# Optimization experiments

Measured on AMD Instinct MI355X. Metric: run time of the kernel, lower is better.

The kernel has to match this reference:

```python
import jax, jax.numpy as jnp
import numpy as np

K = 20      # kNN neighbours (hardcoded in DGCNN)
RES = 64    # 3D grid resolution


def setup_inputs() -> dict:
    key = jax.random.key(0)
    k1, k2 = jax.random.split(key)
    pts = jax.random.uniform(k1, (4, 4096, 3), dtype=jnp.float32)    # point coords in (0,1)
    query = jax.random.uniform(k2, (4, 8192, 3), dtype=jnp.float32)  # query coords in (0,1)
    return {"pts": pts, "query": query}


def _graph_feature(pts, k):
    # pts: (B, N, 3). Faithful to knn() + get_graph_feature(): topk of negative
    # squared pairwise distance (includes self), gather neighbours, cat(nbr - x, x),
    # then max-pool over the k neighbours (standard EdgeConv reduction).
    sq = jnp.sum(pts * pts, axis=-1)                          # (B, N)
    inner = jnp.einsum('bnd,bmd->bnm', pts, pts)              # (B, N, N)
    neg_dist = 2.0 * inner - sq[:, :, None] - sq[:, None, :]  # -||xi - xj||^2
    _, idx = jax.lax.top_k(neg_dist, k)                       # (B, N, k)
    nbr = jax.vmap(lambda p, i: p[i])(pts, idx)               # (B, N, k, 3) gather
    central = jnp.broadcast_to(pts[:, :, None, :], nbr.shape)
    feat = jnp.concatenate([nbr - central, central], axis=-1)  # (B, N, k, 6)
    return jnp.max(feat, axis=2)                               # (B, N, 6)


def _corners(pts, res):
    # Trilinear corner indices and weights, faithful to point_rasterize / grid_interp.
    size = jnp.float32(res)
    ind0 = jnp.floor(pts * size).astype(jnp.int32)                       # (B, P, 3)
    ind1 = jnp.mod(jnp.ceil(pts * size), size).astype(jnp.int32)         # wrap-around
    com = jnp.stack(jnp.meshgrid(*([jnp.arange(2)] * 3), indexing='ij'),
                    axis=-1).reshape(-1, 3)                              # (8, 3) corner combos
    pick1 = (com[None, None] != 0)                                       # (1, 1, 8, 3)
    ind_n = jnp.where(pick1, ind1[:, :, None, :], ind0[:, :, None, :])   # (B, P, 8, 3)
    xyz0 = ind0.astype(pts.dtype) / size
    xyz1 = (ind0.astype(pts.dtype) + 1.0) / size
    # opposite corner position (torch: xyz01[1 - com_])
    pos_opp = jnp.where(pick1, xyz0[:, :, None, :], xyz1[:, :, None, :])
    w = jnp.prod(jnp.abs(pts[:, :, None, :] - pos_opp) * size, axis=-1)  # (B, P, 8)
    return ind_n, w


def _rasterize(pts, vals, res):
    # pts: (B, N, 3), vals: (B, N, F) -> grid (B, res, res, res, F) via scatter-add.
    B, _, F = vals.shape
    ind_n, w = _corners(pts, res)
    flat = (ind_n[..., 0] * res + ind_n[..., 1]) * res + ind_n[..., 2]   # (B, N, 8)
    contrib = w[..., None] * vals[:, :, None, :]                          # (B, N, 8, F)

    def one(fl, c):
        return jnp.zeros((res * res * res, F), vals.dtype).at[fl.reshape(-1)].add(
            c.reshape(-1, F))

    grid = jax.vmap(one)(flat, contrib)                                   # (B, res^3, F)
    return grid.reshape(B, res, res, res, F)


def _grid_interp(grid, q, res):
    # grid: (B, res, res, res, F), q: (B, M, 3) -> (B, M, F)
    ind_n, w = _corners(q, res)

    def one(g, i):
        return g[i[..., 0], i[..., 1], i[..., 2]]   # (M, 8, F) gather

    lat = jax.vmap(one)(grid, ind_n)
    return jnp.sum(lat * w[..., None], axis=-2)


def reference(pts, query):
    feat = _graph_feature(pts, K)            # (B, N, 6)  kNN graph-feature gather
    grid = _rasterize(pts, feat, RES)        # (B, R, R, R, 6) trilinear scatter
    out = _grid_interp(grid, query, RES)     # (B, M, 6)  trilinear gather
    return out
```

## Files before the change

kernel.cpp:

```cpp
#include <hip/hip_runtime.h>

#define BATCH 4
#define NPTS  4096
#define NQ    8192
#define KNN   20
#define RES   64
#define FDIM  6
#define BN    (BATCH * NPTS)

#define WPB   16
#define CAP   128
#define R0 0.1551f

#define GRID_ELEMS ((size_t)BATCH * RES * RES * RES * FDIM)
#define GRID_BYTES (GRID_ELEMS * sizeof(float))

__device__ __forceinline__ float dist2s(float cx, float cy, float cz,
                                        float px, float py, float pz) {
    float dx = cx - px, dy = cy - py, dz = cz - pz;
    return __builtin_fmaf(dz, dz, __builtin_fmaf(dy, dy, dx * dx));
}

__global__ __launch_bounds__(1024) void knn_kernel(const float* __restrict__ pts,
                                                   float* __restrict__ feat) {
    __shared__ float sh[NPTS * 3];
    __shared__ float cd2[WPB][CAP];
    __shared__ unsigned short cidx[WPB][CAP];

    const int tid  = threadIdx.x;
    const int w    = tid >> 6;
    const int lane = tid & 63;
    const int pgrp = blockIdx.x % (NPTS / WPB);
    const int b    = blockIdx.x / (NPTS / WPB);
    const int pi   = pgrp * WPB + w;
    const int pt   = b * NPTS + pi;

    {
        const float4* src = (const float4*)(pts + (size_t)b * NPTS * 3);
        float4* dst = (float4*)sh;
        dst[tid]        = src[tid];
        dst[tid + 1024] = src[tid + 1024];
        dst[tid + 2048] = src[tid + 2048];
    }
    __syncthreads();

    const float px = sh[pi * 3 + 0];
    const float py = sh[pi * 3 + 1];
    const float pz = sh[pi * 3 + 2];

    float r = R0;
    #pragma unroll
    for (int it = 0; it < 2; ++it) {
        float ex = fminf(px + r, 1.f) - fmaxf(px - r, 0.f);
        float ey = fminf(py + r, 1.f) - fmaxf(py - r, 0.f);
        float ez = fminf(pz + r, 1.f) - fmaxf(pz - r, 0.f);
        float frac = (ex * ey * ez) / (8.f * r * r * r);
        r = R0 * __powf(frac, -1.f / 3.f);
    }
    r *= 1.05f;
    const float tau = r * r;

    float*          wd2 = cd2[w];
    unsigned short* wid = cidx[w];
    int total = 0;
    for (int it = 0; it < 64; ++it) {
        const int j = (it << 6) + lane;
        float d2 = dist2s(sh[j * 3 + 0], sh[j * 3 + 1], sh[j * 3 + 2], px, py, pz);
        bool pred = d2 <= tau;
        unsigned long long m = __ballot(pred);
        int before = __builtin_amdgcn_mbcnt_hi((unsigned)(m >> 32),
                     __builtin_amdgcn_mbcnt_lo((unsigned)m, 0));
        int slot = total + before;
        if (pred && slot < CAP) { wd2[slot] = d2; wid[slot] = (unsigned short)j; }
        total += __popcll(m);
    }

    float gx = -3.4e38f, gy = -3.4e38f, gz = -3.4e38f;
    const bool ok = (total >= KNN) && (total <= CAP);

    if (ok) {
        unsigned u0 = (lane < total)      ? __float_as_uint(wd2[lane])      : 0x7F800000u;
        unsigned u1 = (lane + 64 < total) ? __float_as_uint(wd2[lane + 64]) : 0x7F800000u;
        unsigned lo = 0u, hi = __float_as_uint(tau);
        while (lo < hi) {
            unsigned mid = (lo + hi) >> 1;
            int c = __popcll(__ballot(u0 <= mid)) + __popcll(__ballot(u1 <= mid));
            if (c >= KNN) hi = mid; else lo = mid + 1;
        }
        const unsigned tb = hi;
        if (u0 <= tb) {
            int j = wid[lane];
            gx = fmaxf(gx, sh[j * 3 + 0]); gy = fmaxf(gy, sh[j * 3 + 1]); gz = fmaxf(gz, sh[j * 3 + 2]);
        }
        if (u1 <= tb) {
            int j = wid[lane + 64];
            gx = fmaxf(gx, sh[j * 3 + 0]); gy = fmaxf(gy, sh[j * 3 + 1]); gz = fmaxf(gz, sh[j * 3 + 2]);
        }
    } else {
        unsigned lo = 0u, hi = 0x7F7FFFFFu;
        while (lo < hi) {
            unsigned mid = (lo + hi) >> 1;
            int c = 0;
            for (int it = 0; it < 64; ++it) {
                const int j = (it << 6) + lane;
                float d2 = dist2s(sh[j * 3 + 0], sh[j * 3 + 1], sh[j * 3 + 2], px, py, pz);
                c += __popcll(__ballot(__float_as_uint(d2) <= mid));
            }
            if (c >= KNN) hi = mid; else lo = mid + 1;
        }
        const unsigned tb = hi;
        for (int it = 0; it < 64; ++it) {
            const int j = (it << 6) + lane;
            float d2 = dist2s(sh[j * 3 + 0], sh[j * 3 + 1], sh[j * 3 + 2], px, py, pz);
            if (__float_as_uint(d2) <= tb) {
                gx = fmaxf(gx, sh[j * 3 + 0]); gy = fmaxf(gy, sh[j * 3 + 1]); gz = fmaxf(gz, sh[j * 3 + 2]);
            }
        }
    }

    #pragma unroll
    for (int dlt = 1; dlt < 64; dlt <<= 1) {
        gx = fmaxf(gx, __shfl_xor(gx, dlt, 64));
        gy = fmaxf(gy, __shfl_xor(gy, dlt, 64));
        gz = fmaxf(gz, __shfl_xor(gz, dlt, 64));
    }

    if (lane == 0) {
        float* f = feat + (size_t)pt * FDIM;
        f[0] = gx - px; f[1] = gy - py; f[2] = gz - pz;
        f[3] = px; f[4] = py; f[5] = pz;
    }
}

__device__ __forceinline__ void corner_setup(float px, float py, float pz,
                                             int i0[3], int i1[3],
                                             float w0[3], float w1[3]) {
    float p[3] = {px, py, pz};
    #pragma unroll
    for (int d = 0; d < 3; ++d) {
        float f  = p[d] * 64.0f;
        float fl = floorf(f);
        i0[d] = (int)fl;
        i1[d] = ((int)ceilf(f)) & (RES - 1);
        float x0 = fl / 64.0f;
        float x1 = (fl + 1.0f) / 64.0f;
        w0[d] = fabsf(p[d] - x1) * 64.0f;
        w1[d] = fabsf(p[d] - x0) * 64.0f;
    }
}

__global__ __launch_bounds__(256) void rasterize_kernel(const float* __restrict__ pts,
                                                        const float* __restrict__ feat,
                                                        float* __restrict__ grid) {
    int gid = blockIdx.x * 256 + threadIdx.x;
    int pid = gid >> 3;
    int c   = gid & 7;
    int b   = pid / NPTS;

    const float* p = pts + (size_t)pid * 3;
    float px = p[0], py = p[1], pz = p[2];

    int i0[3], i1[3];
    float w0[3], w1[3];
    corner_setup(px, py, pz, i0, i1, w0, w1);

    int bx = (c >> 2) & 1, by = (c >> 1) & 1, bz = c & 1;
    int ix = bx ? i1[0] : i0[0];
    int iy = by ? i1[1] : i0[1];
    int iz = bz ? i1[2] : i0[2];
    float w = (bx ? w1[0] : w0[0]) * (by ? w1[1] : w0[1]) * (bz ? w1[2] : w0[2]);

    const float* f = feat + (size_t)pid * FDIM;
    float* gb = grid + (size_t)b * RES * RES * RES * FDIM
                     + ((size_t)(ix * RES + iy) * RES + iz) * FDIM;
    #pragma unroll
    for (int ch = 0; ch < FDIM; ++ch)
        atomicAdd(&gb[ch], w * f[ch]);
}

__global__ __launch_bounds__(256) void interp_kernel(const float* __restrict__ query,
                                                     const float* __restrict__ grid,
                                                     float* __restrict__ out) {
    int gid = blockIdx.x * 256 + threadIdx.x;
    int qid = gid >> 3;
    int c   = gid & 7;
    int b   = qid / NQ;

    const float* q = query + (size_t)qid * 3;
    float qx = q[0], qy = q[1], qz = q[2];

    int i0[3], i1[3];
    float w0[3], w1[3];
    corner_setup(qx, qy, qz, i0, i1, w0, w1);

    int bx = (c >> 2) & 1, by = (c >> 1) & 1, bz = c & 1;
    int ix = bx ? i1[0] : i0[0];
    int iy = by ? i1[1] : i0[1];
    int iz = bz ? i1[2] : i0[2];
    float w = (bx ? w1[0] : w0[0]) * (by ? w1[1] : w0[1]) * (bz ? w1[2] : w0[2]);

    const float2* g = (const float2*)(grid + (size_t)b * RES * RES * RES * FDIM
                                           + ((size_t)(ix * RES + iy) * RES + iz) * FDIM);
    float2 g0 = g[0], g1 = g[1], g2 = g[2];
    float acc[FDIM] = { w * g0.x, w * g0.y, w * g1.x, w * g1.y, w * g2.x, w * g2.y };

    #pragma unroll
    for (int delta = 1; delta < 8; delta <<= 1) {
        #pragma unroll
        for (int ch = 0; ch < FDIM; ++ch)
            acc[ch] += __shfl_xor(acc[ch], delta, 64);
    }

    if ((threadIdx.x & 7) == 0) {
        float2* o = (float2*)(out + (size_t)qid * FDIM);
        o[0] = make_float2(acc[0], acc[1]);
        o[1] = make_float2(acc[2], acc[3]);
        o[2] = make_float2(acc[4], acc[5]);
    }
}

extern "C" void kernel_launch(void* const* d_in, const int* in_sizes, int n_in,
                              void* d_out, int out_size, void* d_ws, size_t ws_size,
                              hipStream_t stream) {
    const float* pts   = (const float*)d_in[0];
    const float* query = (const float*)d_in[1];
    float* out = (float*)d_out;

    float* grid = (float*)d_ws;
    float* feat = (float*)d_out;

    hipMemsetAsync(grid, 0, GRID_BYTES, stream);

    knn_kernel<<<BN / WPB, 1024, 0, stream>>>(pts, feat);

    rasterize_kernel<<<(BN * 8) / 256, 256, 0, stream>>>(pts, feat, grid);
    interp_kernel<<<(BATCH * NQ * 8) / 256, 256, 0, stream>>>(query, grid, out);
}
```

Baseline: 138.7 us.

## Use SoA shared layout, two-point-per-lane scan, and branchless packed candidate writes

Point coordinates in shared memory move from an interleaved xyz array to three separate per-axis arrays, so each lane reads float2 pairs and handles two candidates per iteration with an unrolled loop. Candidate distance and index are packed into one uint2 entry. Out-of-radius lanes write to a dummy buffer instead of taking a conditional store. The aim is fewer LDS instructions and less divergence in the kNN radius scan. In exchange the global-to-shared load becomes a strided scalar loop instead of float4 copies, and every lane now does two LDS stores per iteration.

Measured after the change: 138.5 us. Within noise of the previous version (-0.1%).

```diff
diff --git a/kernel.cpp b/kernel.cpp
--- a/kernel.cpp
+++ b/kernel.cpp
@@ -21,11 +21,18 @@
     return __builtin_fmaf(dz, dz, __builtin_fmaf(dy, dy, dx * dx));
 }
 
+__device__ __forceinline__ int mbcnt64(unsigned long long m) {
+    return __builtin_amdgcn_mbcnt_hi((unsigned)(m >> 32),
+           __builtin_amdgcn_mbcnt_lo((unsigned)m, 0));
+}
+
 __global__ __launch_bounds__(1024) void knn_kernel(const float* __restrict__ pts,
                                                    float* __restrict__ feat) {
-    __shared__ float sh[NPTS * 3];
-    __shared__ float cd2[WPB][CAP];
-    __shared__ unsigned short cidx[WPB][CAP];
+    __shared__ float sxf[NPTS];
+    __shared__ float syf[NPTS];
+    __shared__ float szf[NPTS];
+    __shared__ uint2 went[WPB][CAP];
+    __shared__ uint2 dump[64];
 
     const int tid  = threadIdx.x;
     const int w    = tid >> 6;
@@ -36,17 +43,16 @@
     const int pt   = b * NPTS + pi;
 
     {
-        const float4* src = (const float4*)(pts + (size_t)b * NPTS * 3);
-        float4* dst = (float4*)sh;
-        dst[tid]        = src[tid];
-        dst[tid + 1024] = src[tid + 1024];
-        dst[tid + 2048] = src[tid + 2048];
+        const float* src = pts + (size_t)b * NPTS * 3;
+        for (int i = tid; i < NPTS; i += 1024) {
+            sxf[i] = src[i * 3 + 0];
+            syf[i] = src[i * 3 + 1];
+            szf[i] = src[i * 3 + 2];
+        }
     }
     __syncthreads();
 
-    const float px = sh[pi * 3 + 0];
-    const float py = sh[pi * 3 + 1];
-    const float pz = sh[pi * 3 + 2];
+    const float px = sxf[pi], py = syf[pi], pz = szf[pi];
 
     float r = R0;
     #pragma unroll
@@ -60,27 +66,39 @@
     r *= 1.05f;
     const float tau = r * r;
 
-    float*          wd2 = cd2[w];
-    unsigned short* wid = cidx[w];
+    const float2* vx = (const float2*)sxf;
+    const float2* vy = (const float2*)syf;
+    const float2* vz = (const float2*)szf;
+    uint2* we = went[w];
     int total = 0;
-    for (int it = 0; it < 64; ++it) {
-        const int j = (it << 6) + lane;
-        float d2 = dist2s(sh[j * 3 + 0], sh[j * 3 + 1], sh[j * 3 + 2], px, py, pz);
-        bool pred = d2 <= tau;
-        unsigned long long m = __ballot(pred);
-        int before = __builtin_amdgcn_mbcnt_hi((unsigned)(m >> 32),
-                     __builtin_amdgcn_mbcnt_lo((unsigned)m, 0));
-        int slot = total + before;
-        if (pred && slot < CAP) { wd2[slot] = d2; wid[slot] = (unsigned short)j; }
-        total += __popcll(m);
+
+    #pragma unroll 4
+    for (int it = 0; it < 32; ++it) {
+        const int i2 = (it << 6) + lane;
+        float2 cx = vx[i2], cy = vy[i2], cz = vz[i2];
+        float da = dist2s(cx.x, cy.x, cz.x, px, py, pz);
+        float db = dist2s(cx.y, cy.y, cz.y, px, py, pz);
+        bool pa = da <= tau, pb = db <= tau;
+        unsigned long long ma = __ballot(pa);
+        unsigned long long mb = __ballot(pb);
+        int cnta = __popcll(ma);
+        int sa = total + mbcnt64(ma);
+        int sb = total + cnta + mbcnt64(mb);
+        uint2* aa = (pa && sa < CAP) ? &we[sa] : &dump[lane];
+        *aa = make_uint2(__float_as_uint(da), (unsigned)(2 * i2));
+        uint2* ab = (pb && sb < CAP) ? &we[sb] : &dump[lane];
+        *ab = make_uint2(__float_as_uint(db), (unsigned)(2 * i2 + 1));
+        total += cnta + __popcll(mb);
     }
 
     float gx = -3.4e38f, gy = -3.4e38f, gz = -3.4e38f;
     const bool ok = (total >= KNN) && (total <= CAP);
 
     if (ok) {
-        unsigned u0 = (lane < total)      ? __float_as_uint(wd2[lane])      : 0x7F800000u;
-        unsigned u1 = (lane + 64 < total) ? __float_as_uint(wd2[lane + 64]) : 0x7F800000u;
+        uint2 e0 = we[lane];
+        uint2 e1 = we[lane + 64];
+        unsigned u0 = (lane < total)      ? e0.x : 0x7F800000u;
+        unsigned u1 = (lane + 64 < total) ? e1.x : 0x7F800000u;
         unsigned lo = 0u, hi = __float_as_uint(tau);
         while (lo < hi) {
             unsigned mid = (lo + hi) >> 1;
@@ -89,12 +107,12 @@
         }
         const unsigned tb = hi;
         if (u0 <= tb) {
-            int j = wid[lane];
-            gx = fmaxf(gx, sh[j * 3 + 0]); gy = fmaxf(gy, sh[j * 3 + 1]); gz = fmaxf(gz, sh[j * 3 + 2]);
+            int j = e0.y;
+            gx = fmaxf(gx, sxf[j]); gy = fmaxf(gy, syf[j]); gz = fmaxf(gz, szf[j]);
         }
         if (u1 <= tb) {
-            int j = wid[lane + 64];
-            gx = fmaxf(gx, sh[j * 3 + 0]); gy = fmaxf(gy, sh[j * 3 + 1]); gz = fmaxf(gz, sh[j * 3 + 2]);
+            int j = e1.y;
+            gx = fmaxf(gx, sxf[j]); gy = fmaxf(gy, syf[j]); gz = fmaxf(gz, szf[j]);
         }
     } else {
         unsigned lo = 0u, hi = 0x7F7FFFFFu;
@@ -103,7 +121,7 @@
             int c = 0;
             for (int it = 0; it < 64; ++it) {
                 const int j = (it << 6) + lane;
-                float d2 = dist2s(sh[j * 3 + 0], sh[j * 3 + 1], sh[j * 3 + 2], px, py, pz);
+                float d2 = dist2s(sxf[j], syf[j], szf[j], px, py, pz);
                 c += __popcll(__ballot(__float_as_uint(d2) <= mid));
             }
             if (c >= KNN) hi = mid; else lo = mid + 1;
@@ -111,9 +129,9 @@
         const unsigned tb = hi;
         for (int it = 0; it < 64; ++it) {
             const int j = (it << 6) + lane;
-            float d2 = dist2s(sh[j * 3 + 0], sh[j * 3 + 1], sh[j * 3 + 2], px, py, pz);
+            float d2 = dist2s(sxf[j], syf[j], szf[j], px, py, pz);
             if (__float_as_uint(d2) <= tb) {
-                gx = fmaxf(gx, sh[j * 3 + 0]); gy = fmaxf(gy, sh[j * 3 + 1]); gz = fmaxf(gz, sh[j * 3 + 2]);
+                gx = fmaxf(gx, sxf[j]); gy = fmaxf(gy, syf[j]); gz = fmaxf(gz, szf[j]);
             }
         }
     }
```
